# Kernel tuning notes

Measured on AMD Instinct MI355X. Metric: run time of the kernel, lower is better.

The kernel has to match this reference:

```python
import jax, jax.numpy as jnp
import numpy as np

EPS = 1e-6

def _ln(x, g, b):
    mu = jnp.mean(x, axis=-1, keepdims=True)
    var = jnp.mean(jnp.square(x - mu), axis=-1, keepdims=True)
    return (x - mu) * jax.lax.rsqrt(var + EPS) * g + b

def setup_inputs() -> dict:
    key = jax.random.key(0)
    ks = jax.random.split(key, 8)
    B, T, D = 4, 4096, 1024
    H = 16
    Dff = 4 * D
    s = 1.0 / np.sqrt(D)
    sf = 1.0 / np.sqrt(Dff)
    return {
        "x": jax.random.normal(ks[0], (B, T, D), dtype=jnp.float32),
        "wq": jax.random.uniform(ks[1], (D, D), jnp.float32, -s, s),
        "wk": jax.random.uniform(ks[2], (D, D), jnp.float32, -s, s),
        "wv": jax.random.uniform(ks[3], (D, D), jnp.float32, -s, s),
        "wo": jax.random.uniform(ks[4], (D, D), jnp.float32, -s, s),
        "ln1_g": jnp.ones((D,), jnp.float32),
        "ln1_b": jnp.zeros((D,), jnp.float32),
        "w1": jax.random.uniform(ks[5], (D, Dff), jnp.float32, -s, s),
        "b1": jnp.zeros((Dff,), jnp.float32),
        "w2": jax.random.uniform(ks[6], (Dff, D), jnp.float32, -sf, sf),
        "b2": jnp.zeros((D,), jnp.float32),
        "ln2_g": jnp.ones((D,), jnp.float32),
        "ln2_b": jnp.zeros((D,), jnp.float32),
    }

def reference(x, wq, wk, wv, wo, ln1_g, ln1_b, w1, b1, w2, b2, ln2_g, ln2_b):
    B, T, D = x.shape
    H = 16
    dk = D // H
    x1 = _ln(x, ln1_g, ln1_b)
    q = (x1 @ wq).reshape(B, T, H, dk)
    k = (x1 @ wk).reshape(B, T, H, dk)
    v = (x1 @ wv).reshape(B, T, H, dk)
    # NOTE: faithful to source -- attention mixes HEADS at each token position
    # attn[b,t,h,g] = softmax_g( sum_d q[b,t,h,d]*k[b,t,g,d] / sqrt(dk) )
    attn = jax.nn.softmax(jnp.einsum('bthd,btgd->bthg', q / np.sqrt(dk), k), axis=-1)
    o = jnp.einsum('bthg,btgd->bthd', attn, v)
    # faithful head-major reshape: transpose(1,2).contiguous().view(B,T,-1)
    o = jnp.transpose(o, (0, 2, 1, 3)).reshape(B, T, H * dk)
    o = o @ wo
    q2 = _ln(o + x, ln1_g, ln1_b)  # same layer_norm params reused
    h = jax.nn.gelu(q2 @ w1 + b1, approximate=False)
    y = h @ w2 + b2 + q2
    return _ln(y, ln2_g, ln2_b)
```

## Files before the change

kernel.cpp:

```cpp
#include <hip/hip_runtime.h>


typedef __attribute__((ext_vector_type(8))) short s16x8;
typedef __attribute__((ext_vector_type(4))) short s16x4;
typedef __attribute__((ext_vector_type(4))) float f32x4;

__device__ __forceinline__ short f2bf(float x) {
  unsigned u = __builtin_bit_cast(unsigned, x);
  u = (u + 0x7FFFu + ((u >> 16) & 1u)) >> 16;
  return (short)u;
}
__device__ __forceinline__ float bf2f(short s) {
  unsigned u = ((unsigned)(unsigned short)s) << 16;
  return __builtin_bit_cast(float, u);
}

__device__ __forceinline__ void ld_g2l16(const short* g, const short* l) {
  __builtin_amdgcn_global_load_lds(
      (const __attribute__((address_space(1))) void*)g,
      (__attribute__((address_space(3))) void*)l, 16, 0, 0);
}

__device__ __forceinline__ s16x8 lds_read8(const short* smem, int off) {
  const __attribute__((address_space(3))) short* p =
      (const __attribute__((address_space(3))) short*)smem;
  return *(const __attribute__((address_space(3))) s16x8*)(p + off);
}

__device__ __forceinline__ float fast_gelu(float v) {
  float y = 0.7978845608f * (v + 0.044715f * v * v * v);
  float ay = fabsf(y);
  float t = __expf(-2.0f * ay);
  float th = (1.0f - t) * __frcp_rn(1.0f + t);
  th = (y >= 0.f) ? th : -th;
  return 0.5f * v * (1.0f + th);
}

#define MFMA16(va, vb, vc) \
  __builtin_amdgcn_mfma_f32_16x16x32_bf16(va, vb, vc, 0, 0, 0)

template <int EPI>
__global__ __launch_bounds__(512, 2) void gemm256(
    const short* __restrict__ A, const short* __restrict__ BT,
    void* __restrict__ outp, const float* __restrict__ bias, int N, int K) {
  extern __shared__ __align__(16) short smem[];

  const int t = threadIdx.x;
  const int lane = t & 63, w = t >> 6;
  const int wm = w >> 2, wn = w & 3;

  const int nbn = N >> 8;
  const int oi = (int)blockIdx.x;
  const int seq = oi >> 3;
  const int bq = seq / nbn;
  const int bm = (oi & 7) * 8 + bq;
  const int bn = seq - bq * nbn;

  const int l8 = lane >> 3;
  const int lcw = ((lane & 7) ^ l8) * 8;
  const short* gA = A + (size_t)(bm * 256 + w * 8 + l8) * K + lcw;
  const short* gB = BT + (size_t)(bn * 256 + w * 8 + l8) * K + lcw;
  const int lb = w * 512;

  auto stage = [&](const short* g, int bufo, int h, int kt) {
    const int go = h * 128 * K + kt * 64;
    ld_g2l16(g + go, smem + bufo + h * 8192 + lb);
    ld_g2l16(g + go + 64 * K, smem + bufo + h * 8192 + 4096 + lb);
  };

  const int fr = lane & 15, fc = lane >> 4;
  const int baseA = (wm * 128 + fr) * 64;
  const int baseB = (wn * 64 + fr) * 64;
  const int sl0 = (fc ^ (fr & 7)) * 8;
  const int sl1 = ((4 + fc) ^ (fr & 7)) * 8;

  f32x4 acc[8][4];
#pragma unroll
  for (int m = 0; m < 8; ++m)
#pragma unroll
    for (int n = 0; n < 4; ++n) acc[m][n] = (f32x4){0.f, 0.f, 0.f, 0.f};

  const int nt = K >> 6;

  stage(gA, 0, 0, 0);
  stage(gA, 0, 1, 0);
  stage(gB, 32768, 0, 0);
  stage(gB, 32768, 1, 0);
  if (nt > 1) {
    stage(gA, 16384, 0, 1);
    stage(gA, 16384, 1, 1);
    stage(gB, 49152, 0, 1);
    stage(gB, 49152, 1, 1);
    asm volatile("s_waitcnt vmcnt(8)" ::: "memory");
  } else {
    asm volatile("s_waitcnt vmcnt(0)" ::: "memory");
  }
  __builtin_amdgcn_s_barrier();
  asm volatile("" ::: "memory");

  for (int u = 0; u < nt; ++u) {
    const bool pf = (u + 2 < nt);
    const int pa = (u & 1) << 14;
    const int pb = 32768 + pa;

    s16x8 a0[4][2], a1[4][2], b0[2][2], b1[2][2];
#pragma unroll
    for (int mi = 0; mi < 4; ++mi) {
      a0[mi][0] = lds_read8(smem, pa + baseA + mi * 1024 + sl0);
      a0[mi][1] = lds_read8(smem, pa + baseA + mi * 1024 + sl1);
    }
#pragma unroll
    for (int ni = 0; ni < 2; ++ni) {
      b0[ni][0] = lds_read8(smem, pb + baseB + ni * 1024 + sl0);
      b0[ni][1] = lds_read8(smem, pb + baseB + ni * 1024 + sl1);
    }
#pragma unroll
    for (int ni = 0; ni < 2; ++ni) {
      b1[ni][0] = lds_read8(smem, pb + baseB + 2048 + ni * 1024 + sl0);
      b1[ni][1] = lds_read8(smem, pb + baseB + 2048 + ni * 1024 + sl1);
    }
#pragma unroll
    for (int mi = 0; mi < 4; ++mi) {
      a1[mi][0] = lds_read8(smem, pa + baseA + 4096 + mi * 1024 + sl0);
      a1[mi][1] = lds_read8(smem, pa + baseA + 4096 + mi * 1024 + sl1);
    }

    __builtin_amdgcn_s_setprio(1);
#pragma unroll
    for (int mi = 0; mi < 4; ++mi)
#pragma unroll
      for (int ni = 0; ni < 2; ++ni) {
        acc[mi][ni] = MFMA16(a0[mi][0], b0[ni][0], acc[mi][ni]);
        acc[mi][ni] = MFMA16(a0[mi][1], b0[ni][1], acc[mi][ni]);
      }
#pragma unroll
    for (int mi = 0; mi < 4; ++mi)
#pragma unroll
      for (int ni = 0; ni < 2; ++ni) {
        acc[mi][2 + ni] = MFMA16(a0[mi][0], b1[ni][0], acc[mi][2 + ni]);
        acc[mi][2 + ni] = MFMA16(a0[mi][1], b1[ni][1], acc[mi][2 + ni]);
      }
#pragma unroll
    for (int mi = 0; mi < 4; ++mi)
#pragma unroll
      for (int ni = 0; ni < 2; ++ni) {
        acc[4 + mi][2 + ni] = MFMA16(a1[mi][0], b1[ni][0], acc[4 + mi][2 + ni]);
        acc[4 + mi][2 + ni] = MFMA16(a1[mi][1], b1[ni][1], acc[4 + mi][2 + ni]);
      }
    __builtin_amdgcn_s_setprio(0);

    asm volatile("s_waitcnt lgkmcnt(0)" ::: "memory");
    __builtin_amdgcn_s_barrier();
    asm volatile("" ::: "memory");

    if (pf) {
      stage(gB, pb, 0, u + 2);
      stage(gB, pb, 1, u + 2);
      stage(gA, pa, 0, u + 2);
      stage(gA, pa, 1, u + 2);
    }

    __builtin_amdgcn_s_setprio(1);
#pragma unroll
    for (int mi = 0; mi < 4; ++mi)
#pragma unroll
      for (int ni = 0; ni < 2; ++ni) {
        acc[4 + mi][ni] = MFMA16(a1[mi][0], b0[ni][0], acc[4 + mi][ni]);
        acc[4 + mi][ni] = MFMA16(a1[mi][1], b0[ni][1], acc[4 + mi][ni]);
      }
    __builtin_amdgcn_s_setprio(0);

    if (pf) {
      asm volatile("s_waitcnt vmcnt(8)" ::: "memory");
    } else {
      asm volatile("s_waitcnt vmcnt(0)" ::: "memory");
    }
    __builtin_amdgcn_s_barrier();
    asm volatile("" ::: "memory");
  }

  const int mb = bm * 256 + wm * 128;
  const int nb = bn * 256 + wn * 64;
  const int cr = (lane >> 4) * 4;
  const int cc = lane & 15;
#pragma unroll
  for (int m = 0; m < 8; ++m) {
#pragma unroll
    for (int n = 0; n < 4; ++n) {
#pragma unroll
      for (int r = 0; r < 4; ++r) {
        const size_t row = (size_t)(mb + m * 16 + cr + r);
        const size_t col = (size_t)(nb + n * 16 + cc);
        float v = acc[m][n][r];
        if constexpr (EPI == 0) {
          ((short*)outp)[row * N + col] = f2bf(v);
        } else if constexpr (EPI == 1) {
          ((float*)outp)[row * N + col] = v;
        } else if constexpr (EPI == 2) {
          v += bias[col];
          ((short*)outp)[row * N + col] = f2bf(fast_gelu(v));
        } else {
          float prev = ((float*)outp)[row * N + col];
          v += prev;
          if (bias) v += bias[col];
          ((float*)outp)[row * N + col] = v;
        }
      }
    }
  }
}

template <int EPI>
__global__ __launch_bounds__(512, 4) void gemm128(
    const short* __restrict__ A, const short* __restrict__ BT,
    void* __restrict__ outp, const float* __restrict__ bias, int N, int K) {
  extern __shared__ __align__(16) short smem[];

  const int t = threadIdx.x;
  const int lane = t & 63, w = t >> 6;
  const int wm = w >> 2, wn = w & 3;

  const int nbn = N >> 8;
  const int oi = (int)blockIdx.x;
  const int seq = oi >> 3;
  const int bq = seq / nbn;
  const int bm = (oi & 7) * 16 + bq;
  const int bn = seq - bq * nbn;

  const int lr = lane >> 2;
  const int lc = ((lane & 3) - ((lane >> 3) & 3)) & 3;
  const short* gA = A + (size_t)(bm * 128 + lr) * K + lc * 8;
  const short* gB = BT + (size_t)(bn * 256 + lr) * K + lc * 8;

  auto stageA = [&](int par, int kt) {
    ld_g2l16(gA + (size_t)(w * 16) * K + kt * 32, smem + par + w * 512);
  };
  auto stageB = [&](int par, int kt) {
    ld_g2l16(gB + (size_t)(2 * w * 16) * K + kt * 32,
             smem + par + 2 * w * 512);
    ld_g2l16(gB + (size_t)((2 * w + 1) * 16) * K + kt * 32,
             smem + par + (2 * w + 1) * 512);
  };

  const int fr = lane & 15, fc = lane >> 4;
  const int sl = ((fc + (fr >> 1)) & 3) * 8;
  const int baseA = (wm * 64 + fr) * 32 + sl;
  const int baseB = (wn * 64 + fr) * 32 + sl;

  f32x4 acc[4][4];
#pragma unroll
  for (int m = 0; m < 4; ++m)
#pragma unroll
    for (int n = 0; n < 4; ++n) acc[m][n] = (f32x4){0.f, 0.f, 0.f, 0.f};

  const int nt = K >> 5;

  stageA(0, 0);
  stageB(8192, 0);
  stageA(4096, 1);
  stageB(16384, 1);
  asm volatile("s_waitcnt vmcnt(3)" ::: "memory");
  __builtin_amdgcn_s_barrier();
  asm volatile("" ::: "memory");

  for (int u = 0; u < nt; ++u) {
    const bool pf = (u + 2 < nt);
    const int pA = (u & 1) * 4096;
    const int pB = 8192 + (u & 1) * 8192;

    s16x8 a[4], b[4];
#pragma unroll
    for (int i = 0; i < 4; ++i) a[i] = lds_read8(smem, pA + baseA + i * 512);
#pragma unroll
    for (int i = 0; i < 4; ++i) b[i] = lds_read8(smem, pB + baseB + i * 512);
    asm volatile("s_waitcnt lgkmcnt(0)" ::: "memory");
    __builtin_amdgcn_s_barrier();
    asm volatile("" ::: "memory");

    if (pf) {
      stageA(pA, u + 2);
      stageB(pB, u + 2);
    }
    __builtin_amdgcn_s_setprio(1);
#pragma unroll
    for (int mi = 0; mi < 4; ++mi)
#pragma unroll
      for (int ni = 0; ni < 4; ++ni)
        acc[mi][ni] = MFMA16(a[mi], b[ni], acc[mi][ni]);
    __builtin_amdgcn_s_setprio(0);
    if (pf) {
      asm volatile("s_waitcnt vmcnt(3)" ::: "memory");
    } else {
      asm volatile("s_waitcnt vmcnt(0)" ::: "memory");
    }
    __builtin_amdgcn_s_barrier();
    asm volatile("" ::: "memory");
  }

  const int mb = bm * 128 + wm * 64;
  const int nb = bn * 256 + wn * 64;
  const int cr = (lane >> 4) * 4;
  const int cc = lane & 15;
#pragma unroll
  for (int m = 0; m < 4; ++m) {
#pragma unroll
    for (int n = 0; n < 4; ++n) {
#pragma unroll
      for (int r = 0; r < 4; ++r) {
        const size_t row = (size_t)(mb + m * 16 + cr + r);
        const size_t col = (size_t)(nb + n * 16 + cc);
        float v = acc[m][n][r];
        if constexpr (EPI == 0) {
          ((short*)outp)[row * N + col] = f2bf(v);
        } else if constexpr (EPI == 1) {
          ((float*)outp)[row * N + col] = v;
        } else if constexpr (EPI == 2) {
          v += bias[col];
          ((short*)outp)[row * N + col] = f2bf(fast_gelu(v));
        } else {
          float prev = ((float*)outp)[row * N + col];
          v += prev;
          if (bias) v += bias[col];
          ((float*)outp)[row * N + col] = v;
        }
      }
    }
  }
}

__global__ __launch_bounds__(256) void ln_k(
    const float* __restrict__ in, const float* __restrict__ add,
    const float* __restrict__ g, const float* __restrict__ b,
    float* __restrict__ outf, short* __restrict__ outb) {
  const int row = blockIdx.x;
  const size_t off = (size_t)row * 1024;
  const int t = threadIdx.x;
  float4 v = ((const float4*)(in + off))[t];
  if (add) {
    float4 w = ((const float4*)(add + off))[t];
    v.x += w.x; v.y += w.y; v.z += w.z; v.w += w.w;
  }
  float s = v.x + v.y + v.z + v.w;
  float ss = v.x * v.x + v.y * v.y + v.z * v.z + v.w * v.w;
#pragma unroll
  for (int o = 32; o > 0; o >>= 1) {
    s += __shfl_xor(s, o, 64);
    ss += __shfl_xor(ss, o, 64);
  }
  __shared__ float ps[4], pss[4];
  const int lane = t & 63, wave = t >> 6;
  if (lane == 0) { ps[wave] = s; pss[wave] = ss; }
  __syncthreads();
  s = ps[0] + ps[1] + ps[2] + ps[3];
  ss = pss[0] + pss[1] + pss[2] + pss[3];
  const float mean = s * (1.0f / 1024.0f);
  const float var = ss * (1.0f / 1024.0f) - mean * mean;
  const float rstd = rsqrtf(var + 1e-6f);
  const float4 gv = ((const float4*)g)[t];
  const float4 bv = ((const float4*)b)[t];
  float4 o4;
  o4.x = (v.x - mean) * rstd * gv.x + bv.x;
  o4.y = (v.y - mean) * rstd * gv.y + bv.y;
  o4.z = (v.z - mean) * rstd * gv.z + bv.z;
  o4.w = (v.w - mean) * rstd * gv.w + bv.w;
  if (outf) ((float4*)(outf + off))[t] = o4;
  if (outb) {
    s16x4 ob;
    ob[0] = f2bf(o4.x); ob[1] = f2bf(o4.y);
    ob[2] = f2bf(o4.z); ob[3] = f2bf(o4.w);
    *(s16x4*)(outb + off + t * 4) = ob;
  }
}

__device__ __forceinline__ void wconv_tile(const float* __restrict__ W,
                                           short* __restrict__ WT, int K,
                                           int N, int n0, int k0,
                                           float (*tile)[33], int c, int r) {
#pragma unroll
  for (int rr = r; rr < 32; rr += 8)
    tile[rr][c] = W[(size_t)(k0 + rr) * N + n0 + c];
  __syncthreads();
#pragma unroll
  for (int rr = r; rr < 32; rr += 8)
    WT[(size_t)(n0 + rr) * K + k0 + c] = f2bf(tile[c][rr]);
}

__global__ __launch_bounds__(256) void wconv_all(
    const float* __restrict__ wq, const float* __restrict__ wk,
    const float* __restrict__ wv, const float* __restrict__ wo,
    const float* __restrict__ w1, const float* __restrict__ w2,
    short* __restrict__ WQKVT, short* __restrict__ WOT,
    short* __restrict__ W1T, short* __restrict__ W2aT,
    short* __restrict__ W2bT) {
  __shared__ float tile[32][33];
  const int t = threadIdx.x;
  const int c = t & 31, r = t >> 5;
  const int i = blockIdx.x;
  if (i < 4096) {
    const int seg = i >> 10, j = i & 1023;
    const int n0 = (j & 31) * 32, k0 = (j >> 5) * 32;
    const float* src = (seg == 0) ? wq : (seg == 1) ? wk : (seg == 2) ? wv : wo;
    short* dst = (seg == 3) ? WOT : WQKVT + (size_t)seg * 1024 * 1024;
    wconv_tile(src, dst, 1024, 1024, n0, k0, tile, c, r);
  } else if (i < 8192) {
    const int j = i - 4096;
    const int n0 = (j & 127) * 32, k0 = (j >> 7) * 32;
    wconv_tile(w1, W1T, 1024, 4096, n0, k0, tile, c, r);
  } else if (i < 10240) {
    const int j = i - 8192;
    const int n0 = (j & 31) * 32, k0 = (j >> 5) * 32;
    wconv_tile(w2, W2aT, 2048, 1024, n0, k0, tile, c, r);
  } else {
    const int j = i - 10240;
    const int n0 = (j & 31) * 32, k0 = (j >> 5) * 32;
    wconv_tile(w2 + (size_t)2048 * 1024, W2bT, 2048, 1024, n0, k0, tile, c, r);
  }
}

__global__ __launch_bounds__(256) void attn_k(const short* __restrict__ qkv,
                                              short* __restrict__ omix) {
  __shared__ float Qs[4][16][65];
  __shared__ float Ks[4][16][65];
  __shared__ float Vs[4][16][65];
  __shared__ float Ps[4][16][17];
  const int lane = threadIdx.x & 63;
  const int wave = threadIdx.x >> 6;
  const int tok = blockIdx.x * 4 + wave;
  const short* base = qkv + (size_t)tok * 3072;

#pragma unroll
  for (int half = 0; half < 2; half++) {
    const int e = half * 512 + lane * 8;
    const int h = e >> 6, d = e & 63;
    s16x8 rq = *(const s16x8*)(base + e);
    s16x8 rk = *(const s16x8*)(base + 1024 + e);
    s16x8 rv = *(const s16x8*)(base + 2048 + e);
#pragma unroll
    for (int j = 0; j < 8; j++) {
      Qs[wave][h][d + j] = bf2f(rq[j]);
      Ks[wave][h][d + j] = bf2f(rk[j]);
      Vs[wave][h][d + j] = bf2f(rv[j]);
    }
  }
  __syncthreads();

  const int h = lane & 15;
  const int g0 = (lane >> 4) * 4;
  float sc[4] = {0.f, 0.f, 0.f, 0.f};
  for (int d = 0; d < 64; d++) {
    const float qv = Qs[wave][h][d];
#pragma unroll
    for (int i = 0; i < 4; i++) sc[i] += qv * Ks[wave][g0 + i][d];
  }
#pragma unroll
  for (int i = 0; i < 4; i++) sc[i] *= 0.125f;
  float m = fmaxf(fmaxf(sc[0], sc[1]), fmaxf(sc[2], sc[3]));
  m = fmaxf(m, __shfl_xor(m, 16, 64));
  m = fmaxf(m, __shfl_xor(m, 32, 64));
  float e[4], sum = 0.f;
#pragma unroll
  for (int i = 0; i < 4; i++) { e[i] = __expf(sc[i] - m); sum += e[i]; }
  sum += __shfl_xor(sum, 16, 64);
  sum += __shfl_xor(sum, 32, 64);
  const float inv = __frcp_rn(sum);
#pragma unroll
  for (int i = 0; i < 4; i++) Ps[wave][h][g0 + i] = e[i] * inv;
  __syncthreads();

  const int d0 = (lane >> 4) * 16;
  float o[16];
#pragma unroll
  for (int dd = 0; dd < 16; dd++) o[dd] = 0.f;
  for (int gg = 0; gg < 16; gg++) {
    const float pv = Ps[wave][h][gg];
#pragma unroll
    for (int dd = 0; dd < 16; dd++) o[dd] += pv * Vs[wave][gg][d0 + dd];
  }

  const int b = tok >> 12, t = tok & 4095;
  const size_t dst =
      ((size_t)(b * 4096 + h * 256 + (t >> 4))) * 1024 + (t & 15) * 64 + d0;
  s16x8 w0, w1;
#pragma unroll
  for (int j = 0; j < 8; j++) { w0[j] = f2bf(o[j]); w1[j] = f2bf(o[8 + j]); }
  *(s16x8*)(omix + dst) = w0;
  *(s16x8*)(omix + dst + 8) = w1;
}

extern "C" void kernel_launch(void* const* d_in, const int* in_sizes, int n_in,
                              void* d_out, int out_size, void* d_ws,
                              size_t ws_size, hipStream_t stream) {
  const float* x    = (const float*)d_in[0];
  const float* wq   = (const float*)d_in[1];
  const float* wk   = (const float*)d_in[2];
  const float* wv   = (const float*)d_in[3];
  const float* wo   = (const float*)d_in[4];
  const float* ln1g = (const float*)d_in[5];
  const float* ln1b = (const float*)d_in[6];
  const float* w1   = (const float*)d_in[7];
  const float* b1   = (const float*)d_in[8];
  const float* w2   = (const float*)d_in[9];
  const float* b2   = (const float*)d_in[10];
  const float* ln2g = (const float*)d_in[11];
  const float* ln2b = (const float*)d_in[12];
  float* out = (float*)d_out;

  char* ws = (char*)d_ws;
  const size_t MB = 1024ull * 1024ull;
  const size_t NEEDED = 152 * MB;
  if (ws_size < NEEDED) return;

  short* QKV  = (short*)(ws + 0);
  short* Q2B  = (short*)(ws + 0);
  short* Hbuf = (short*)(ws + 32 * MB);
  short* X1 = (short*)(ws + 96 * MB);
  short* WQKVT = (short*)(ws + 128 * MB);
  short* WOT   = (short*)(ws + 134 * MB);
  short* W1T   = (short*)(ws + 136 * MB);
  short* W2aT  = (short*)(ws + 144 * MB);
  short* W2bT  = (short*)(ws + 148 * MB);

  const dim3 B256(256);
  const dim3 B512(512);
  const unsigned LDS256 = 131072;
  const unsigned LDS128 = 49152;

  static bool attr_done = false;
  if (!attr_done) {
    attr_done = true;
    void (*k0)(const short*, const short*, void*, const float*, int, int) =
        gemm256<0>;
    (void)hipFuncSetAttribute((const void*)k0,
        hipFuncAttributeMaxDynamicSharedMemorySize, (int)LDS256);
    void (*h1)(const short*, const short*, void*, const float*, int, int) =
        gemm128<1>;
    void (*h2)(const short*, const short*, void*, const float*, int, int) =
        gemm128<2>;
    void (*h4)(const short*, const short*, void*, const float*, int, int) =
        gemm128<4>;
    (void)hipFuncSetAttribute((const void*)h1,
        hipFuncAttributeMaxDynamicSharedMemorySize, (int)LDS128);
    (void)hipFuncSetAttribute((const void*)h2,
        hipFuncAttributeMaxDynamicSharedMemorySize, (int)LDS128);
    (void)hipFuncSetAttribute((const void*)h4,
        hipFuncAttributeMaxDynamicSharedMemorySize, (int)LDS128);
  }

  wconv_all<<<dim3(12288), B256, 0, stream>>>(wq, wk, wv, wo, w1, w2, WQKVT,
                                              WOT, W1T, W2aT, W2bT);

  ln_k<<<16384, B256, 0, stream>>>(x, nullptr, ln1g, ln1b, nullptr, X1);

  gemm256<0><<<dim3(768), B512, LDS256, stream>>>(X1, WQKVT, QKV, nullptr,
                                                  3072, 1024);

  attn_k<<<4096, B256, 0, stream>>>(QKV, X1);

  gemm128<1><<<dim3(512), B512, LDS128, stream>>>(X1, WOT, out, nullptr,
                                                  1024, 1024);

  ln_k<<<16384, B256, 0, stream>>>(out, x, ln1g, ln1b, out, Q2B);

  gemm128<2><<<dim3(1024), B512, LDS128, stream>>>(Q2B, W1T, Hbuf, b1,
                                                   2048, 1024);
  gemm128<4><<<dim3(512), B512, LDS128, stream>>>(Hbuf, W2aT, out, nullptr,
                                                  1024, 2048);

  gemm128<2><<<dim3(1024), B512, LDS128, stream>>>(Q2B, W1T + 2048 * 1024,
                                                   Hbuf, b1 + 2048, 2048,
                                                   1024);
  gemm128<4><<<dim3(512), B512, LDS128, stream>>>(Hbuf, W2bT, out, b2,
                                                  1024, 2048);

  ln_k<<<16384, B256, 0, stream>>>(out, nullptr, ln2g, ln2b, out, nullptr);
}
```

Baseline: 799.8 us.

## Triple-buffer LDS in gemm128 to drop per-iteration read barrier

The 128x256 GEMM moves from double to triple buffering of A and B tiles in LDS, rotating three 12288-element stages. Prefetch for step u+2 is issued at the top of the iteration into the buffer last read two steps ago, which removes the barrier that separated LDS reads from the next global-to-LDS loads. Each iteration now needs one barrier instead of two. The cost is 72KB of LDS per block instead of 48KB, which may lower occupancy per CU.

```diff
diff --git a/kernel.cpp b/kernel.cpp
--- a/kernel.cpp
+++ b/kernel.cpp
@@ -232,20 +232,18 @@
   const short* gA = A + (size_t)(bm * 128 + lr) * K + lc * 8;
   const short* gB = BT + (size_t)(bn * 256 + lr) * K + lc * 8;
 
-  auto stageA = [&](int par, int kt) {
+  auto stageT = [&](int par, int kt) {
     ld_g2l16(gA + (size_t)(w * 16) * K + kt * 32, smem + par + w * 512);
-  };
-  auto stageB = [&](int par, int kt) {
     ld_g2l16(gB + (size_t)(2 * w * 16) * K + kt * 32,
-             smem + par + 2 * w * 512);
+             smem + par + 4096 + 2 * w * 512);
     ld_g2l16(gB + (size_t)((2 * w + 1) * 16) * K + kt * 32,
-             smem + par + (2 * w + 1) * 512);
+             smem + par + 4096 + (2 * w + 1) * 512);
   };
 
   const int fr = lane & 15, fc = lane >> 4;
   const int sl = ((fc + (fr >> 1)) & 3) * 8;
   const int baseA = (wm * 64 + fr) * 32 + sl;
-  const int baseB = (wn * 64 + fr) * 32 + sl;
+  const int baseB = 4096 + (wn * 64 + fr) * 32 + sl;
 
   f32x4 acc[4][4];
 #pragma unroll
@@ -255,32 +253,26 @@
 
   const int nt = K >> 5;
 
-  stageA(0, 0);
-  stageB(8192, 0);
-  stageA(4096, 1);
-  stageB(16384, 1);
+  stageT(0, 0);
+  stageT(12288, 1);
   asm volatile("s_waitcnt vmcnt(3)" ::: "memory");
   __builtin_amdgcn_s_barrier();
   asm volatile("" ::: "memory");
 
+  int pcur = 0, pnxt = 12288, pprv = 24576;
   for (int u = 0; u < nt; ++u) {
     const bool pf = (u + 2 < nt);
-    const int pA = (u & 1) * 4096;
-    const int pB = 8192 + (u & 1) * 8192;
+
+    if (pf) stageT(pprv, u + 2);
 
     s16x8 a[4], b[4];
 #pragma unroll
-    for (int i = 0; i < 4; ++i) a[i] = lds_read8(smem, pA + baseA + i * 512);
-#pragma unroll
-    for (int i = 0; i < 4; ++i) b[i] = lds_read8(smem, pB + baseB + i * 512);
-    asm volatile("s_waitcnt lgkmcnt(0)" ::: "memory");
-    __builtin_amdgcn_s_barrier();
-    asm volatile("" ::: "memory");
-
-    if (pf) {
-      stageA(pA, u + 2);
-      stageB(pB, u + 2);
-    }
+    for (int i = 0; i < 4; ++i)
+      a[i] = lds_read8(smem, pcur + baseA + i * 512);
+#pragma unroll
+    for (int i = 0; i < 4; ++i)
+      b[i] = lds_read8(smem, pcur + baseB + i * 512);
+
     __builtin_amdgcn_s_setprio(1);
 #pragma unroll
     for (int mi = 0; mi < 4; ++mi)
@@ -288,6 +280,8 @@
       for (int ni = 0; ni < 4; ++ni)
         acc[mi][ni] = MFMA16(a[mi], b[ni], acc[mi][ni]);
     __builtin_amdgcn_s_setprio(0);
+
+    asm volatile("s_waitcnt lgkmcnt(0)" ::: "memory");
     if (pf) {
       asm volatile("s_waitcnt vmcnt(3)" ::: "memory");
     } else {
@@ -295,6 +289,11 @@
     }
     __builtin_amdgcn_s_barrier();
     asm volatile("" ::: "memory");
+
+    const int tmp = pcur;
+    pcur = pnxt;
+    pnxt = pprv;
+    pprv = tmp;
   }
 
   const int mb = bm * 128 + wm * 64;
@@ -523,7 +522,7 @@
   const dim3 B256(256);
   const dim3 B512(512);
   const unsigned LDS256 = 131072;
-  const unsigned LDS128 = 49152;
+  const unsigned LDS128 = 73728;
 
   static bool attr_done = false;
   if (!attr_done) {
```

Measured after the change: 776.9 us. -2.9%, faster.
